# Kernel optimization log

Measured on AMD Instinct MI355X. Metric: run time of the kernel, lower is better.

The kernel has to match this reference:

```python
import jax, jax.numpy as jnp
import numpy as np

# Model dims (Gemma-class)
B, T, HID = 1, 3072, 2048
H, KH, D = 16, 8, 128          # q heads, kv heads, head_dim
WIN = 1024                     # sliding window
EPS = 1e-6
SEQ = 1536                     # two packed sequences of length 1536


def _rms(x, w):
    # torch nn.RMSNorm: x * rsqrt(mean(x^2) + eps) [* weight]
    var = jnp.mean(x * x, axis=-1, keepdims=True)
    y = x * jax.lax.rsqrt(var + EPS)
    return y if w is None else y * w


def _rotate_half(x):
    x1, x2 = jnp.split(x, 2, axis=-1)
    return jnp.concatenate([-x2, x1], axis=-1)


def _rope(x, cos, sin):
    # x: [B,T,h,D]; cos/sin: [B,T,rd] -> unsqueeze head dim (matches cos.unsqueeze(2))
    c = cos[:, :, None, :]
    s = sin[:, :, None, :]
    rd = cos.shape[-1]
    xr, xp = x[..., :rd], x[..., rd:]
    xr = xr * c + _rotate_half(xr) * s
    return jnp.concatenate([xr, xp], axis=-1)


def _build_mask(cu_seqlens):
    # causal & within sliding window & same packed sequence (matches _sliding_mask)
    idx = jnp.arange(T)
    seg = jnp.searchsorted(cu_seqlens, idx, side='right') - 1
    i = idx[:, None]
    j = idx[None, :]
    return (i >= j) & ((i - j) < WIN) & (seg[:, None] == seg[None, :])


def _attn_layer(x, wq, qn, k, v, wo, cos, sin, mask):
    # x: [B,T,HID]; k,v: [T,KH,D] (possibly shared from an earlier layer)
    q = _rope(_rms((x @ wq).reshape(B, T, H, D), qn), cos, sin).reshape(T, H, D)
    rep = H // k.shape[1]
    kk = jnp.repeat(k, rep, axis=1)   # GQA: repeat_interleave over head dim
    vv = jnp.repeat(v, rep, axis=1)
    s = jnp.einsum('qhd,khd->hqk', q, kk)          # scale = 1.0 (as in source)
    s = jnp.where(mask, s, jnp.asarray(-1e30, s.dtype))
    p = jax.nn.softmax(s, axis=-1)
    o = jnp.einsum('hqk,khd->qhd', p, vv).reshape(B, T, H * D)
    return o @ wo


def setup_inputs() -> dict:
    key = jax.random.key(0)
    ks = jax.random.split(key, 10)
    hidden_states = jax.random.normal(ks[0], (B, T, HID), jnp.float32)
    # RoPE tables with per-packed-sequence position resets
    pos = jnp.concatenate([jnp.arange(SEQ), jnp.arange(SEQ)]).astype(jnp.float32)
    inv = 1.0 / (10000.0 ** (jnp.arange(0, D, 2, dtype=jnp.float32) / D))
    fr = pos[:, None] * inv[None, :]
    emb = jnp.concatenate([fr, fr], axis=-1)     # [T, D]
    cos = jnp.cos(emb)[None]                     # [1, T, D]
    sin = jnp.sin(emb)[None]
    w = lambda k, sh: 0.02 * jax.random.normal(k, sh, jnp.float32)
    return {
        'hidden_states': hidden_states,
        'cos': cos, 'sin': sin,
        'wq0': w(ks[1], (HID, H * D)), 'wk0': w(ks[2], (HID, KH * D)),
        'wv0': w(ks[3], (HID, KH * D)), 'wo0': w(ks[4], (H * D, HID)),
        'qn0': 1.0 + 0.01 * jax.random.normal(ks[5], (D,), jnp.float32),
        'kn0': 1.0 + 0.01 * jax.random.normal(ks[6], (D,), jnp.float32),
        'wq1': w(ks[7], (HID, H * D)), 'wo1': w(ks[8], (H * D, HID)),
        'qn1': 1.0 + 0.01 * jax.random.normal(ks[9], (D,), jnp.float32),
        'cu_seqlens': jnp.array([0, SEQ, T], dtype=jnp.int32),
    }


def reference(hidden_states, cos, sin, wq0, wk0, wv0, wo0, qn0, kn0, wq1, wo1, qn1, cu_seqlens):
    mask = _build_mask(cu_seqlens)
    # Layer 0: source layer -> computes and stores K/V
    k = _rope(_rms((hidden_states @ wk0).reshape(B, T, KH, D), kn0), cos, sin).reshape(T, KH, D)
    v = _rms((hidden_states @ wv0).reshape(B, T, KH, D), None).reshape(T, KH, D)
    out0 = _attn_layer(hidden_states, wq0, qn0, k, v, wo0, cos, sin, mask)
    # Layer 1: KV-shared layer -> reuses layer 0's K/V (skips k/v projections)
    out1 = _attn_layer(out0, wq1, qn1, k, v, wo1, cos, sin, mask)
    return out1
```

## Files before the change

kernel.cpp:

```cpp
#include <hip/hip_runtime.h>
#include <hip/hip_bf16.h>

#define T_TOK 3072
#define HIDDEN 2048
#define NHQ 16
#define NHKV 8
#define DH 128
#define WINDOW 1024
#define KVN 1024

typedef __attribute__((ext_vector_type(4))) float f32x4;
typedef __attribute__((ext_vector_type(8))) short bf16x8;
typedef __attribute__((ext_vector_type(8))) unsigned short ushort8;
typedef __attribute__((ext_vector_type(4))) unsigned short ushort4v;

__device__ __forceinline__ unsigned short f2bf(float f) {
  union { float fv; unsigned u; } v; v.fv = f;
  unsigned r = v.u + 0x7fffu + ((v.u >> 16) & 1u);
  return (unsigned short)(r >> 16);
}
__device__ __forceinline__ float bf2f(unsigned short h) {
  union { unsigned u; float f; } v; v.u = ((unsigned)h) << 16;
  return v.f;
}
__device__ __forceinline__ void split2(float f, unsigned short& hi, unsigned short& lo) {
  hi = f2bf(f);
  lo = f2bf(f - bf2f(hi));
}

__global__ __launch_bounds__(256) void cvt_split(const float* __restrict__ x,
                                                 unsigned short* __restrict__ yh,
                                                 unsigned short* __restrict__ yl, int n) {
  int i = (blockIdx.x * 256 + threadIdx.x) * 4;
  if (i >= n) return;
  f32x4 v = *(const f32x4*)(x + i);
  ushort4v oh, ol;
#pragma unroll
  for (int j = 0; j < 4; ++j) {
    unsigned short h, l;
    split2(v[j], h, l);
    oh[j] = h; ol[j] = l;
  }
  *(ushort4v*)(yh + i) = oh;
  *(ushort4v*)(yl + i) = ol;
}

__global__ __launch_bounds__(256) void transpose_qkv(const float* __restrict__ wq0,
                                                     const float* __restrict__ wk0,
                                                     const float* __restrict__ wv0,
                                                     unsigned short* __restrict__ Wth,
                                                     unsigned short* __restrict__ Wtl) {
  __shared__ float tile[32][33];
  const int K = HIDDEN;
  int id = blockIdx.x;
  const float* W; int N, local; size_t dstoff;
  if (id < 4096)      { W = wq0; N = 2048; local = id;        dstoff = 0; }
  else if (id < 6144) { W = wk0; N = 1024; local = id - 4096; dstoff = (size_t)2048 * K; }
  else                { W = wv0; N = 1024; local = id - 6144; dstoff = (size_t)3072 * K; }
  int ntc = N / 32;
  int bn = (local % ntc) * 32, bk = (local / ntc) * 32;
  int tx = threadIdx.x & 31, ty = threadIdx.x >> 5;
#pragma unroll
  for (int i = 0; i < 4; ++i)
    tile[ty + i * 8][tx] = W[(size_t)(bk + ty + i * 8) * N + bn + tx];
  __syncthreads();
#pragma unroll
  for (int i = 0; i < 4; ++i) {
    unsigned short h, l;
    split2(tile[tx][ty + i * 8], h, l);
    Wth[dstoff + (size_t)(bn + ty + i * 8) * K + bk + tx] = h;
    Wtl[dstoff + (size_t)(bn + ty + i * 8) * K + bk + tx] = l;
  }
}

__global__ __launch_bounds__(256) void transpose_w_split(const float* __restrict__ W,
                                                         unsigned short* __restrict__ Wth,
                                                         unsigned short* __restrict__ Wtl,
                                                         int K, int N) {
  __shared__ float tile[32][33];
  int bn = blockIdx.x * 32, bk = blockIdx.y * 32;
  int tx = threadIdx.x & 31, ty = threadIdx.x >> 5;
#pragma unroll
  for (int i = 0; i < 4; ++i)
    tile[ty + i * 8][tx] = W[(size_t)(bk + ty + i * 8) * N + bn + tx];
  __syncthreads();
#pragma unroll
  for (int i = 0; i < 4; ++i) {
    unsigned short h, l;
    split2(tile[tx][ty + i * 8], h, l);
    Wth[(size_t)(bn + ty + i * 8) * K + bk + tx] = h;
    if (Wtl) Wtl[(size_t)(bn + ty + i * 8) * K + bk + tx] = l;
  }
}

__global__ __launch_bounds__(256) void transpose_u16(const unsigned short* __restrict__ src,
                                                     unsigned short* __restrict__ dst,
                                                     int R, int C) {
  __shared__ unsigned short tile[32][33];
  int bc = blockIdx.x * 32, br = blockIdx.y * 32;
  int tx = threadIdx.x & 31, ty = threadIdx.x >> 5;
#pragma unroll
  for (int i = 0; i < 4; ++i)
    tile[ty + i * 8][tx] = src[(size_t)(br + ty + i * 8) * C + bc + tx];
  __syncthreads();
#pragma unroll
  for (int i = 0; i < 4; ++i)
    dst[(size_t)(bc + ty + i * 8) * R + br + tx] = tile[tx][ty + i * 8];
}

#define GSLOT(lane) ((((lane) & 3) + 4 - (((lane) >> 3) & 3)) & 3)

template <int OUT>
__global__ __launch_bounds__(256) void gemm3_128(const unsigned short* __restrict__ Ah,
                                                 const unsigned short* __restrict__ Al,
                                                 const unsigned short* __restrict__ Bh,
                                                 const unsigned short* __restrict__ Bl,
                                                 float* __restrict__ Cq,
                                                 float* __restrict__ Ckv,
                                                 unsigned short* __restrict__ Ch,
                                                 unsigned short* __restrict__ Cl,
                                                 int strd, int M, int N, int K) {
  __shared__ unsigned short ah_lds[128 * 32];
  __shared__ unsigned short al_lds[128 * 32];
  __shared__ unsigned short bh_lds[128 * 32];
  __shared__ unsigned short bl_lds[128 * 32];
  const int tid = threadIdx.x, lane = tid & 63, wave = tid >> 6;
  const int wr = (wave >> 1) * 64, wc = (wave & 1) * 64;
  const int g = lane >> 4, r16 = lane & 15;
  int nwg = gridDim.x * gridDim.y;
  int id = blockIdx.y * gridDim.x + blockIdx.x;
  int nid = (id & 7) * (nwg >> 3) + (id >> 3);
  const int bm = nid % gridDim.x, bn = nid / gridDim.x;
  f32x4 acc[4][4];
#pragma unroll
  for (int i = 0; i < 4; ++i)
#pragma unroll
    for (int j = 0; j < 4; ++j) acc[i][j] = (f32x4){0.f, 0.f, 0.f, 0.f};

  const unsigned short* AhB = Ah + (size_t)bm * 128 * K;
  const unsigned short* AlB = Al + (size_t)bm * 128 * K;
  const unsigned short* BhB = Bh + (size_t)bn * 128 * K;
  const unsigned short* BlB = Bl + (size_t)bn * 128 * K;

  const int slg = GSLOT(lane) * 8;
  const int sr = ((r16 >> 1) & 3);

  for (int kt = 0; kt < K; kt += 32) {
    __syncthreads();
#pragma unroll
    for (int c = 0; c < 2; ++c) {
      size_t goff = (size_t)(wave * 32 + c * 16 + (lane >> 2)) * K + kt + slg;
      int loff = (wave * 2 + c) * 512;
      __builtin_amdgcn_global_load_lds(
          (const __attribute__((address_space(1))) unsigned int*)(AhB + goff),
          (__attribute__((address_space(3))) unsigned int*)(ah_lds + loff), 16, 0, 0);
      __builtin_amdgcn_global_load_lds(
          (const __attribute__((address_space(1))) unsigned int*)(AlB + goff),
          (__attribute__((address_space(3))) unsigned int*)(al_lds + loff), 16, 0, 0);
      __builtin_amdgcn_global_load_lds(
          (const __attribute__((address_space(1))) unsigned int*)(BhB + goff),
          (__attribute__((address_space(3))) unsigned int*)(bh_lds + loff), 16, 0, 0);
      __builtin_amdgcn_global_load_lds(
          (const __attribute__((address_space(1))) unsigned int*)(BlB + goff),
          (__attribute__((address_space(3))) unsigned int*)(bl_lds + loff), 16, 0, 0);
    }
    __syncthreads();
    bf16x8 ahf[4], alf[4], bhf[4], blf[4];
    int sa = ((g + sr) & 3) * 8;
#pragma unroll
    for (int i = 0; i < 4; ++i) {
      ahf[i] = *(const bf16x8*)&ah_lds[(wr + i * 16 + r16) * 32 + sa];
      alf[i] = *(const bf16x8*)&al_lds[(wr + i * 16 + r16) * 32 + sa];
      bhf[i] = *(const bf16x8*)&bh_lds[(wc + i * 16 + r16) * 32 + sa];
      blf[i] = *(const bf16x8*)&bl_lds[(wc + i * 16 + r16) * 32 + sa];
    }
#pragma unroll
    for (int i = 0; i < 4; ++i)
#pragma unroll
      for (int j = 0; j < 4; ++j) {
        acc[i][j] = __builtin_amdgcn_mfma_f32_16x16x32_bf16(ahf[i], bhf[j], acc[i][j], 0, 0, 0);
        acc[i][j] = __builtin_amdgcn_mfma_f32_16x16x32_bf16(ahf[i], blf[j], acc[i][j], 0, 0, 0);
        acc[i][j] = __builtin_amdgcn_mfma_f32_16x16x32_bf16(alf[i], bhf[j], acc[i][j], 0, 0, 0);
      }
  }

#pragma unroll
  for (int i = 0; i < 4; ++i) {
    int row = bm * 128 + wr + i * 16 + g * 4;
#pragma unroll
    for (int j = 0; j < 4; ++j) {
      int colg = bn * 128 + wc + j * 16 + r16;
      if (OUT == 0) {
        float* Cb; int cc;
        if (colg < 2048) { Cb = Cq; cc = colg; } else { Cb = Ckv; cc = colg - 2048; }
#pragma unroll
        for (int r = 0; r < 4; ++r)
          Cb[(size_t)(row + r) * strd + cc] = acc[i][j][r];
      } else {
#pragma unroll
        for (int r = 0; r < 4; ++r) {
          unsigned short h, l;
          split2(acc[i][j][r], h, l);
          Ch[(size_t)(row + r) * N + colg] = h;
          Cl[(size_t)(row + r) * N + colg] = l;
        }
      }
    }
  }
}

__global__ __launch_bounds__(256) void gemm3_96(const unsigned short* __restrict__ Ah,
                                                const unsigned short* __restrict__ Al,
                                                const unsigned short* __restrict__ Bh,
                                                const unsigned short* __restrict__ Bl,
                                                float* __restrict__ Cf,
                                                int M, int N, int K) {
  __shared__ unsigned short ah_lds[96 * 32];
  __shared__ unsigned short al_lds[96 * 32];
  __shared__ unsigned short bh_lds[128 * 32];
  __shared__ unsigned short bl_lds[128 * 32];
  const int tid = threadIdx.x, lane = tid & 63, wave = tid >> 6;
  const int wr = (wave >> 1) * 48, wc = (wave & 1) * 64;
  const int g = lane >> 4, r16 = lane & 15;
  int nwg = gridDim.x * gridDim.y;
  int id = blockIdx.y * gridDim.x + blockIdx.x;
  int nid = (id & 7) * (nwg >> 3) + (id >> 3);
  const int bm = nid % gridDim.x, bn = nid / gridDim.x;
  f32x4 acc[3][4];
#pragma unroll
  for (int i = 0; i < 3; ++i)
#pragma unroll
    for (int j = 0; j < 4; ++j) acc[i][j] = (f32x4){0.f, 0.f, 0.f, 0.f};

  const unsigned short* AhB = Ah + (size_t)bm * 96 * K;
  const unsigned short* AlB = Al + (size_t)bm * 96 * K;
  const unsigned short* BhB = Bh + (size_t)bn * 128 * K;
  const unsigned short* BlB = Bl + (size_t)bn * 128 * K;

  const int slg = GSLOT(lane) * 8;
  const int sr = ((r16 >> 1) & 3);

  for (int kt = 0; kt < K; kt += 32) {
    __syncthreads();
    {
      int c = wave;
      size_t goff = (size_t)(c * 16 + (lane >> 2)) * K + kt + slg;
      __builtin_amdgcn_global_load_lds(
          (const __attribute__((address_space(1))) unsigned int*)(AhB + goff),
          (__attribute__((address_space(3))) unsigned int*)(ah_lds + c * 512), 16, 0, 0);
      __builtin_amdgcn_global_load_lds(
          (const __attribute__((address_space(1))) unsigned int*)(AlB + goff),
          (__attribute__((address_space(3))) unsigned int*)(al_lds + c * 512), 16, 0, 0);
      if (wave < 2) {
        int c2 = 4 + wave;
        size_t goff2 = (size_t)(c2 * 16 + (lane >> 2)) * K + kt + slg;
        __builtin_amdgcn_global_load_lds(
            (const __attribute__((address_space(1))) unsigned int*)(AhB + goff2),
            (__attribute__((address_space(3))) unsigned int*)(ah_lds + c2 * 512), 16, 0, 0);
        __builtin_amdgcn_global_load_lds(
            (const __attribute__((address_space(1))) unsigned int*)(AlB + goff2),
            (__attribute__((address_space(3))) unsigned int*)(al_lds + c2 * 512), 16, 0, 0);
      }
    }
#pragma unroll
    for (int c = 0; c < 2; ++c) {
      size_t goff = (size_t)(wave * 32 + c * 16 + (lane >> 2)) * K + kt + slg;
      int loff = (wave * 2 + c) * 512;
      __builtin_amdgcn_global_load_lds(
          (const __attribute__((address_space(1))) unsigned int*)(BhB + goff),
          (__attribute__((address_space(3))) unsigned int*)(bh_lds + loff), 16, 0, 0);
      __builtin_amdgcn_global_load_lds(
          (const __attribute__((address_space(1))) unsigned int*)(BlB + goff),
          (__attribute__((address_space(3))) unsigned int*)(bl_lds + loff), 16, 0, 0);
    }
    __syncthreads();
    bf16x8 ahf[3], alf[3], bhf[4], blf[4];
    int sa = ((g + sr) & 3) * 8;
#pragma unroll
    for (int i = 0; i < 3; ++i) {
      ahf[i] = *(const bf16x8*)&ah_lds[(wr + i * 16 + r16) * 32 + sa];
      alf[i] = *(const bf16x8*)&al_lds[(wr + i * 16 + r16) * 32 + sa];
    }
#pragma unroll
    for (int j = 0; j < 4; ++j) {
      bhf[j] = *(const bf16x8*)&bh_lds[(wc + j * 16 + r16) * 32 + sa];
      blf[j] = *(const bf16x8*)&bl_lds[(wc + j * 16 + r16) * 32 + sa];
    }
#pragma unroll
    for (int i = 0; i < 3; ++i)
#pragma unroll
      for (int j = 0; j < 4; ++j) {
        acc[i][j] = __builtin_amdgcn_mfma_f32_16x16x32_bf16(ahf[i], bhf[j], acc[i][j], 0, 0, 0);
        acc[i][j] = __builtin_amdgcn_mfma_f32_16x16x32_bf16(ahf[i], blf[j], acc[i][j], 0, 0, 0);
        acc[i][j] = __builtin_amdgcn_mfma_f32_16x16x32_bf16(alf[i], bhf[j], acc[i][j], 0, 0, 0);
      }
  }

#pragma unroll
  for (int i = 0; i < 3; ++i) {
    int row = bm * 96 + wr + i * 16 + g * 4;
#pragma unroll
    for (int j = 0; j < 4; ++j) {
      int col = bn * 128 + wc + j * 16 + r16;
#pragma unroll
      for (int r = 0; r < 4; ++r)
        Cf[(size_t)(row + r) * N + col] = acc[i][j][r];
    }
  }
}

__global__ __launch_bounds__(256) void gemm1_96(const unsigned short* __restrict__ Ah,
                                                const unsigned short* __restrict__ Bh,
                                                float* __restrict__ Cf,
                                                int M, int N, int K) {
  __shared__ unsigned short ah_lds[96 * 32];
  __shared__ unsigned short bh_lds[128 * 32];
  const int tid = threadIdx.x, lane = tid & 63, wave = tid >> 6;
  const int wr = (wave >> 1) * 48, wc = (wave & 1) * 64;
  const int g = lane >> 4, r16 = lane & 15;
  int nwg = gridDim.x * gridDim.y;
  int id = blockIdx.y * gridDim.x + blockIdx.x;
  int nid = (id & 7) * (nwg >> 3) + (id >> 3);
  const int bm = nid % gridDim.x, bn = nid / gridDim.x;
  f32x4 acc[3][4];
#pragma unroll
  for (int i = 0; i < 3; ++i)
#pragma unroll
    for (int j = 0; j < 4; ++j) acc[i][j] = (f32x4){0.f, 0.f, 0.f, 0.f};

  const unsigned short* AhB = Ah + (size_t)bm * 96 * K;
  const unsigned short* BhB = Bh + (size_t)bn * 128 * K;

  const int slg = GSLOT(lane) * 8;
  const int sr = ((r16 >> 1) & 3);

  for (int kt = 0; kt < K; kt += 32) {
    __syncthreads();
    {
      int c = wave;
      size_t goff = (size_t)(c * 16 + (lane >> 2)) * K + kt + slg;
      __builtin_amdgcn_global_load_lds(
          (const __attribute__((address_space(1))) unsigned int*)(AhB + goff),
          (__attribute__((address_space(3))) unsigned int*)(ah_lds + c * 512), 16, 0, 0);
      if (wave < 2) {
        int c2 = 4 + wave;
        size_t goff2 = (size_t)(c2 * 16 + (lane >> 2)) * K + kt + slg;
        __builtin_amdgcn_global_load_lds(
            (const __attribute__((address_space(1))) unsigned int*)(AhB + goff2),
            (__attribute__((address_space(3))) unsigned int*)(ah_lds + c2 * 512), 16, 0, 0);
      }
    }
#pragma unroll
    for (int c = 0; c < 2; ++c) {
      size_t goff = (size_t)(wave * 32 + c * 16 + (lane >> 2)) * K + kt + slg;
      __builtin_amdgcn_global_load_lds(
          (const __attribute__((address_space(1))) unsigned int*)(BhB + goff),
          (__attribute__((address_space(3))) unsigned int*)(bh_lds + (wave * 2 + c) * 512), 16, 0, 0);
    }
    __syncthreads();
    bf16x8 ahf[3], bhf[4];
    int sa = ((g + sr) & 3) * 8;
#pragma unroll
    for (int i = 0; i < 3; ++i)
      ahf[i] = *(const bf16x8*)&ah_lds[(wr + i * 16 + r16) * 32 + sa];
#pragma unroll
    for (int j = 0; j < 4; ++j)
      bhf[j] = *(const bf16x8*)&bh_lds[(wc + j * 16 + r16) * 32 + sa];
#pragma unroll
    for (int i = 0; i < 3; ++i)
#pragma unroll
      for (int j = 0; j < 4; ++j)
        acc[i][j] = __builtin_amdgcn_mfma_f32_16x16x32_bf16(ahf[i], bhf[j], acc[i][j], 0, 0, 0);
  }

#pragma unroll
  for (int i = 0; i < 3; ++i) {
    int row = bm * 96 + wr + i * 16 + g * 4;
#pragma unroll
    for (int j = 0; j < 4; ++j) {
      int col = bn * 128 + wc + j * 16 + r16;
#pragma unroll
      for (int r = 0; r < 4; ++r)
        Cf[(size_t)(row + r) * N + col] = acc[i][j][r];
    }
  }
}

__global__ __launch_bounds__(256) void rms_kv(const float* __restrict__ X,
                                              const float* __restrict__ kn,
                                              const float* __restrict__ cosp,
                                              const float* __restrict__ sinp,
                                              unsigned short* __restrict__ kh,
                                              unsigned short* __restrict__ kl,
                                              unsigned short* __restrict__ vh) {
  const int half = T_TOK * NHKV / 4;
  bool isV = (int)blockIdx.x >= half;
  int bid = isV ? blockIdx.x - half : blockIdx.x;
  int row = bid * 4 + (threadIdx.x >> 6);
  int lane = threadIdx.x & 63;
  int t = row >> 3, hh_ = row & 7;
  const float* x = X + (size_t)t * HIDDEN + (isV ? KVN : 0) + (size_t)hh_ * DH;
  float x1 = x[lane], x2 = x[lane + 64];
  float ss = x1 * x1 + x2 * x2;
#pragma unroll
  for (int m = 1; m < 64; m <<= 1) ss += __shfl_xor(ss, m, 64);
  float inv = rsqrtf(ss * (1.0f / 128.0f) + 1e-6f);
  float y1 = x1 * inv, y2 = x2 * inv;
  if (!isV) {
    y1 *= kn[lane]; y2 *= kn[lane + 64];
    float c1 = cosp[t * DH + lane], s1 = sinp[t * DH + lane];
    float c2 = cosp[t * DH + lane + 64], s2 = sinp[t * DH + lane + 64];
    float o1 = y1 * c1 - y2 * s1;
    float o2 = y2 * c2 + y1 * s2;
    unsigned short h, l;
    split2(o1, h, l);
    kh[(size_t)row * DH + lane] = h;
    kl[(size_t)row * DH + lane] = l;
    split2(o2, h, l);
    kh[(size_t)row * DH + lane + 64] = h;
    kl[(size_t)row * DH + lane + 64] = l;
  } else {
    vh[(size_t)row * DH + lane] = f2bf(y1);
    vh[(size_t)row * DH + lane + 64] = f2bf(y2);
  }
}

template <int WRITE_LO>
__global__ __launch_bounds__(384) void attn3(const float* __restrict__ Qf,
                                             const float* __restrict__ qnw,
                                             const float* __restrict__ cosp,
                                             const float* __restrict__ sinp,
                                             const unsigned short* __restrict__ Kh,
                                             const unsigned short* __restrict__ Kl,
                                             const unsigned short* __restrict__ Vth,
                                             unsigned short* __restrict__ Oh,
                                             unsigned short* __restrict__ Ol,
                                             const int* __restrict__ cu, int ncu) {
  __shared__ unsigned short kh_lds[32][136];
  __shared__ unsigned short kl_lds[32][136];
  __shared__ unsigned short vh_lds[144][40];
  __shared__ unsigned short ph_lds[6][16][40];

  int id = blockIdx.y * gridDim.x + blockIdx.x;
  int nid = (id & 7) * 64 + (id >> 3);
  const int qt = nid & 31, h = nid >> 5;
  const int qbase = qt * 96;
  const int kvh = h >> 1;
  const int tid = threadIdx.x, lane = tid & 63, wave = tid >> 6;
  const int g = lane >> 4, r16 = lane & 15;

  for (int i = tid; i < 16 * 40; i += 384) {
    int rr = i / 40, cc = i % 40;
    vh_lds[128 + rr][cc] = (rr == 0) ? (unsigned short)0x3F80 : (unsigned short)0;
  }

  bf16x8 aqh[4], aql[4];
  {
    int q_r = qbase + wave * 16 + r16;
    const float* xq = Qf + (size_t)q_r * HIDDEN + h * DH;
    float xv[4][8];
    float ss = 0.f;
#pragma unroll
    for (int ks = 0; ks < 4; ++ks) {
      f32x4 a = *(const f32x4*)(xq + ks * 32 + g * 8);
      f32x4 b = *(const f32x4*)(xq + ks * 32 + g * 8 + 4);
#pragma unroll
      for (int j = 0; j < 4; ++j) { xv[ks][j] = a[j]; xv[ks][4 + j] = b[j]; }
#pragma unroll
      for (int j = 0; j < 8; ++j) ss += xv[ks][j] * xv[ks][j];
    }
    ss += __shfl_xor(ss, 16, 64);
    ss += __shfl_xor(ss, 32, 64);
    float inv = rsqrtf(ss * (1.0f / 128.0f) + 1e-6f);
    float y[4][8];
#pragma unroll
    for (int ks = 0; ks < 4; ++ks) {
      f32x4 w0 = *(const f32x4*)(qnw + ks * 32 + g * 8);
      f32x4 w1 = *(const f32x4*)(qnw + ks * 32 + g * 8 + 4);
#pragma unroll
      for (int j = 0; j < 4; ++j) {
        y[ks][j] = xv[ks][j] * inv * w0[j];
        y[ks][4 + j] = xv[ks][4 + j] * inv * w1[j];
      }
    }
    const float* cb = cosp + (size_t)q_r * DH;
    const float* sb = sinp + (size_t)q_r * DH;
#pragma unroll
    for (int ks = 0; ks < 4; ++ks) {
      bf16x8 th, tl;
#pragma unroll
      for (int j2 = 0; j2 < 2; ++j2) {
        int col = ks * 32 + g * 8 + j2 * 4;
        f32x4 cv = *(const f32x4*)(cb + col);
        f32x4 sv = *(const f32x4*)(sb + col);
#pragma unroll
        for (int j = 0; j < 4; ++j) {
          float o;
          if (ks < 2) o = y[ks][j2 * 4 + j] * cv[j] - y[ks + 2][j2 * 4 + j] * sv[j];
          else        o = y[ks][j2 * 4 + j] * cv[j] + y[ks - 2][j2 * 4 + j] * sv[j];
          unsigned short hx, lx;
          split2(o, hx, lx);
          th[j2 * 4 + j] = (short)hx;
          tl[j2 * 4 + j] = (short)lx;
        }
      }
      aqh[ks] = th; aql[ks] = tl;
    }
  }

  int ssr[4];
#pragma unroll
  for (int r = 0; r < 4; ++r) {
    int q_r = qbase + wave * 16 + g * 4 + r;
    int s = 0;
    for (int i = 1; i < ncu; ++i) { int v = cu[i]; if (v <= q_r) s = v; }
    ssr[r] = s;
  }
  int ss_base = 0;
  for (int i = 1; i < ncu; ++i) { int v = cu[i]; if (v <= qbase) ss_base = v; }

  float m_r[4] = {-1e30f, -1e30f, -1e30f, -1e30f};
  f32x4 oacc[8];
#pragma unroll
  for (int db = 0; db < 8; ++db) oacc[db] = (f32x4){0.f, 0.f, 0.f, 0.f};
  f32x4 oaccL = (f32x4){0.f, 0.f, 0.f, 0.f};

  int lo = qbase - WINDOW + 1;
  if (lo < ss_base) lo = ss_base;
  if (lo < 0) lo = 0;
  int kt0 = lo & ~31;
  int ktend = qbase + 95;

  const bool stager = tid < 256;
  const int krow = (tid & 255) >> 3, kc = tid & 7;
  const int vd = (tid & 255) >> 1, vhalf = (tid & 1) * 16;
  const int qmin = qbase + wave * 16;
  const int sw0 = ((kc + 2 * (krow & 15)) & 15) * 16;
  const int sw1 = ((kc + 8 + 2 * (krow & 15)) & 15) * 16;

  ushort8 rkh0, rkh1, rkl0, rkl1, rvh0, rvh1;
  auto loadTile = [&](int kt) {
    if (!stager) return;
    size_t goff = ((size_t)(kt + krow) * NHKV + kvh) * DH + kc * 8;
    rkh0 = *(const ushort8*)(Kh + goff);
    rkh1 = *(const ushort8*)(Kh + goff + 64);
    rkl0 = *(const ushort8*)(Kl + goff);
    rkl1 = *(const ushort8*)(Kl + goff + 64);
    size_t voff = ((size_t)kvh * DH + vd) * T_TOK + kt + vhalf;
    rvh0 = *(const ushort8*)(Vth + voff);
    rvh1 = *(const ushort8*)(Vth + voff + 8);
  };
  auto writeTile = [&]() {
    if (!stager) return;
    char* kbh = (char*)&kh_lds[krow][0];
    char* kbl = (char*)&kl_lds[krow][0];
    *(ushort8*)(kbh + sw0) = rkh0;
    *(ushort8*)(kbh + sw1) = rkh1;
    *(ushort8*)(kbl + sw0) = rkl0;
    *(ushort8*)(kbl + sw1) = rkl1;
    *(ushort8*)&vh_lds[vd][vhalf] = rvh0;
    *(ushort8*)&vh_lds[vd][vhalf + 8] = rvh1;
  };

  loadTile(kt0);
  writeTile();
  __syncthreads();

  for (int kt = kt0; kt <= ktend; kt += 32) {
    const bool hasNext = (kt + 32 <= ktend);
    if (hasNext) loadTile(kt + 32);

    f32x4 s0 = (f32x4){0.f, 0.f, 0.f, 0.f}, s1 = (f32x4){0.f, 0.f, 0.f, 0.f};
    {
      const char* kb0h = (const char*)&kh_lds[r16][0];
      const char* kb1h = (const char*)&kh_lds[16 + r16][0];
      const char* kb0l = (const char*)&kl_lds[r16][0];
      const char* kb1l = (const char*)&kl_lds[16 + r16][0];
#pragma unroll
      for (int ks = 0; ks < 4; ++ks) {
        int sl = ((ks * 4 + g + 2 * r16) & 15) * 16;
        bf16x8 bh0 = *(const bf16x8*)(kb0h + sl);
        bf16x8 bh1 = *(const bf16x8*)(kb1h + sl);
        bf16x8 bl0 = *(const bf16x8*)(kb0l + sl);
        bf16x8 bl1 = *(const bf16x8*)(kb1l + sl);
        s0 = __builtin_amdgcn_mfma_f32_16x16x32_bf16(aqh[ks], bh0, s0, 0, 0, 0);
        s0 = __builtin_amdgcn_mfma_f32_16x16x32_bf16(aqh[ks], bl0, s0, 0, 0, 0);
        s0 = __builtin_amdgcn_mfma_f32_16x16x32_bf16(aql[ks], bh0, s0, 0, 0, 0);
        s1 = __builtin_amdgcn_mfma_f32_16x16x32_bf16(aqh[ks], bh1, s1, 0, 0, 0);
        s1 = __builtin_amdgcn_mfma_f32_16x16x32_bf16(aqh[ks], bl1, s1, 0, 0, 0);
        s1 = __builtin_amdgcn_mfma_f32_16x16x32_bf16(aql[ks], bh1, s1, 0, 0, 0);
      }
    }

    float sv0_[4], sv1_[4], mt_[4];
    bool ok0_[4], ok1_[4];
    bool interior = (kt + 31 <= qmin) && (kt >= qmin + 16 - WINDOW) &&
                    __all(kt >= ssr[3]);
    if (interior) {
#pragma unroll
      for (int r = 0; r < 4; ++r) {
        ok0_[r] = ok1_[r] = true;
        sv0_[r] = s0[r]; sv1_[r] = s1[r];
      }
    } else {
#pragma unroll
      for (int r = 0; r < 4; ++r) {
        int q_r = qmin + g * 4 + r;
        int k0 = kt + r16, k1 = k0 + 16;
        ok0_[r] = (k0 <= q_r) && (k0 > q_r - WINDOW) && (k0 >= ssr[r]);
        ok1_[r] = (k1 <= q_r) && (k1 > q_r - WINDOW) && (k1 >= ssr[r]);
        sv0_[r] = ok0_[r] ? s0[r] : -1e30f;
        sv1_[r] = ok1_[r] ? s1[r] : -1e30f;
      }
    }
#pragma unroll
    for (int r = 0; r < 4; ++r) {
      float mt = fmaxf(sv0_[r], sv1_[r]);
#pragma unroll
      for (int mm = 1; mm < 16; mm <<= 1) mt = fmaxf(mt, __shfl_xor(mt, mm, 64));
      mt_[r] = mt;
    }
    float grow = fmaxf(fmaxf(mt_[0] - m_r[0], mt_[1] - m_r[1]),
                       fmaxf(mt_[2] - m_r[2], mt_[3] - m_r[3]));
    if (!__all(grow <= 8.0f)) {
#pragma unroll
      for (int r = 0; r < 4; ++r) {
        float mnew = fmaxf(m_r[r], mt_[r]);
        float alpha = __expf(m_r[r] - mnew);
        m_r[r] = mnew;
#pragma unroll
        for (int db = 0; db < 8; ++db) oacc[db][r] *= alpha;
        oaccL[r] *= alpha;
      }
    }
#pragma unroll
    for (int r = 0; r < 4; ++r) {
      float p0v = ok0_[r] ? __expf(sv0_[r] - m_r[r]) : 0.f;
      float p1v = ok1_[r] ? __expf(sv1_[r] - m_r[r]) : 0.f;
      ph_lds[wave][g * 4 + r][r16] = f2bf(p0v);
      ph_lds[wave][g * 4 + r][16 + r16] = f2bf(p1v);
    }

    bf16x8 pah = *(const bf16x8*)&ph_lds[wave][r16][g * 8];
#pragma unroll
    for (int db = 0; db < 8; ++db) {
      bf16x8 vfh = *(const bf16x8*)&vh_lds[db * 16 + r16][g * 8];
      oacc[db] = __builtin_amdgcn_mfma_f32_16x16x32_bf16(pah, vfh, oacc[db], 0, 0, 0);
    }
    {
      bf16x8 vfo = *(const bf16x8*)&vh_lds[128 + r16][g * 8];
      oaccL = __builtin_amdgcn_mfma_f32_16x16x32_bf16(pah, vfo, oaccL, 0, 0, 0);
    }

    __syncthreads();
    if (hasNext) writeTile();
    __syncthreads();
  }

#pragma unroll
  for (int r = 0; r < 4; ++r) {
    int q_r = qbase + wave * 16 + g * 4 + r;
    float lsum = __shfl(oaccL[r], lane & 48, 64);
    float invl = 1.f / lsum;
#pragma unroll
    for (int db = 0; db < 8; ++db) {
      float ov = oacc[db][r] * invl;
      unsigned short hh, ll;
      split2(ov, hh, ll);
      Oh[(size_t)q_r * (NHQ * DH) + h * DH + db * 16 + r16] = hh;
      if (WRITE_LO) Ol[(size_t)q_r * (NHQ * DH) + h * DH + db * 16 + r16] = ll;
    }
  }
}

extern "C" void kernel_launch(void* const* d_in, const int* in_sizes, int n_in,
                              void* d_out, int out_size, void* d_ws, size_t ws_size,
                              hipStream_t stream) {
  const float* hidden = (const float*)d_in[0];
  const float* cosp   = (const float*)d_in[1];
  const float* sinp   = (const float*)d_in[2];
  const float* wq0    = (const float*)d_in[3];
  const float* wk0    = (const float*)d_in[4];
  const float* wv0    = (const float*)d_in[5];
  const float* wo0    = (const float*)d_in[6];
  const float* qn0    = (const float*)d_in[7];
  const float* kn0    = (const float*)d_in[8];
  const float* wq1    = (const float*)d_in[9];
  const float* wo1    = (const float*)d_in[10];
  const float* qn1    = (const float*)d_in[11];
  const int*   cu     = (const int*)d_in[12];
  int ncu = in_sizes[12];
  (void)n_in; (void)out_size; (void)ws_size;

  const int nX = T_TOK * HIDDEN;

  char* p = (char*)d_ws;
  auto alloc = [&](size_t bytes) { char* r = p; p += (bytes + 255) & ~255ull; return r; };

  float*          c32q  = (float*)alloc((size_t)T_TOK * HIDDEN * 4);
  float*          c32kv = (float*)alloc((size_t)T_TOK * HIDDEN * 4);
  unsigned short* xh    = (unsigned short*)alloc((size_t)T_TOK * HIDDEN * 2);
  unsigned short* xl    = (unsigned short*)alloc((size_t)T_TOK * HIDDEN * 2);
  unsigned short* wth   = (unsigned short*)alloc((size_t)2 * HIDDEN * HIDDEN * 2);
  unsigned short* wtl   = (unsigned short*)alloc((size_t)2 * HIDDEN * HIDDEN * 2);
  unsigned short* kh    = (unsigned short*)alloc((size_t)T_TOK * KVN * 2);
  unsigned short* kl    = (unsigned short*)alloc((size_t)T_TOK * KVN * 2);
  unsigned short* vh    = (unsigned short*)alloc((size_t)T_TOK * KVN * 2);
  unsigned short* vth   = (unsigned short*)alloc((size_t)T_TOK * KVN * 2);

  unsigned short* wo0sh = wth;
  unsigned short* wo0sl = wtl;
  unsigned short* wq1th = wth + (size_t)HIDDEN * HIDDEN;
  unsigned short* wq1tl = wtl + (size_t)HIDDEN * HIDDEN;
  unsigned short* W01th = (unsigned short*)c32q;
  unsigned short* W01tl = W01th + (size_t)HIDDEN * HIDDEN;
  unsigned short* wo1t  = wth;

  cvt_split<<<nX / 1024, 256, 0, stream>>>(hidden, xh, xl, nX);
  transpose_qkv<<<8192, 256, 0, stream>>>(wq0, wk0, wv0, wth, wtl);
  gemm3_128<0><<<dim3(T_TOK / 128, 4096 / 128), 256, 0, stream>>>(
      xh, xl, wth, wtl, c32q, c32kv, nullptr, nullptr, HIDDEN, T_TOK, 4096, HIDDEN);
  cvt_split<<<(HIDDEN * HIDDEN) / 1024, 256, 0, stream>>>(wo0, wo0sh, wo0sl, HIDDEN * HIDDEN);
  transpose_w_split<<<dim3(HIDDEN / 32, HIDDEN / 32), 256, 0, stream>>>(wq1, wq1th, wq1tl, HIDDEN, HIDDEN);
  rms_kv<<<2 * T_TOK * NHKV / 4, 256, 0, stream>>>(c32kv, kn0, cosp, sinp, kh, kl, vh);
  transpose_u16<<<dim3(KVN / 32, T_TOK / 32), 256, 0, stream>>>(vh, vth, T_TOK, KVN);
  attn3<1><<<dim3(32, 16), 384, 0, stream>>>(c32q, qn0, cosp, sinp, kh, kl, vth, xh, xl, cu, ncu);
  gemm3_128<2><<<dim3(HIDDEN / 128, HIDDEN / 128), 256, 0, stream>>>(
      wq1th, wq1tl, wo0sh, wo0sl, nullptr, nullptr, W01th, W01tl, HIDDEN, HIDDEN, HIDDEN, HIDDEN);
  gemm3_96<<<dim3(T_TOK / 96, HIDDEN / 128), 256, 0, stream>>>(
      xh, xl, W01th, W01tl, c32kv, T_TOK, HIDDEN, HIDDEN);
  transpose_w_split<<<dim3(HIDDEN / 32, HIDDEN / 32), 256, 0, stream>>>(wo1, wo1t, nullptr, HIDDEN, HIDDEN);
  attn3<0><<<dim3(32, 16), 384, 0, stream>>>(c32kv, qn1, cosp, sinp, kh, kl, vth, xh, nullptr, cu, ncu);
  gemm1_96<<<dim3(T_TOK / 96, HIDDEN / 128), 256, 0, stream>>>(xh, wo1t, (float*)d_out, T_TOK, HIDDEN, HIDDEN);
}
```

Measured before the change: 668.3 us.

## Fuse weight/input prep kernels, add 64-row GEMM for W01, set MFMA priority

Merges the input split, QKV transpose, wo0 split and wq1 transpose into one prep launch, with a separate workspace for each weight, which cuts launch count and the ordering constraints from aliased buffers. Replaces the 128x128 tile for the 2048x2048 weight-product GEMM with a 64x128 tile, giving more workgroups to fill the CUs. Adds s_setprio around the MFMA loops in attention, and simplifies the wo1 transpose to write only the high bf16 part. The changes are independent and add more kernel code to maintain.

```diff
diff --git a/kernel.cpp b/kernel.cpp
--- a/kernel.cpp
+++ b/kernel.cpp
@@ -28,35 +28,51 @@
   lo = f2bf(f - bf2f(hi));
 }
 
-__global__ __launch_bounds__(256) void cvt_split(const float* __restrict__ x,
-                                                 unsigned short* __restrict__ yh,
-                                                 unsigned short* __restrict__ yl, int n) {
-  int i = (blockIdx.x * 256 + threadIdx.x) * 4;
-  if (i >= n) return;
-  f32x4 v = *(const f32x4*)(x + i);
-  ushort4v oh, ol;
-#pragma unroll
-  for (int j = 0; j < 4; ++j) {
-    unsigned short h, l;
-    split2(v[j], h, l);
-    oh[j] = h; ol[j] = l;
-  }
-  *(ushort4v*)(yh + i) = oh;
-  *(ushort4v*)(yl + i) = ol;
-}
-
-__global__ __launch_bounds__(256) void transpose_qkv(const float* __restrict__ wq0,
-                                                     const float* __restrict__ wk0,
-                                                     const float* __restrict__ wv0,
-                                                     unsigned short* __restrict__ Wth,
-                                                     unsigned short* __restrict__ Wtl) {
+__global__ __launch_bounds__(256) void prep(const float* __restrict__ hidden,
+                                            const float* __restrict__ wq0,
+                                            const float* __restrict__ wk0,
+                                            const float* __restrict__ wv0,
+                                            const float* __restrict__ wo0,
+                                            const float* __restrict__ wq1,
+                                            unsigned short* __restrict__ xh,
+                                            unsigned short* __restrict__ xl,
+                                            unsigned short* __restrict__ wqkvh,
+                                            unsigned short* __restrict__ wqkvl,
+                                            unsigned short* __restrict__ wo0sh,
+                                            unsigned short* __restrict__ wo0sl,
+                                            unsigned short* __restrict__ wq1th,
+                                            unsigned short* __restrict__ wq1tl) {
   __shared__ float tile[32][33];
   const int K = HIDDEN;
   int id = blockIdx.x;
-  const float* W; int N, local; size_t dstoff;
-  if (id < 4096)      { W = wq0; N = 2048; local = id;        dstoff = 0; }
-  else if (id < 6144) { W = wk0; N = 1024; local = id - 4096; dstoff = (size_t)2048 * K; }
-  else                { W = wv0; N = 1024; local = id - 6144; dstoff = (size_t)3072 * K; }
+  if (id < 6144 || (id >= 14336 && id < 18432)) {
+    const float* src; unsigned short *dh, *dl; int local;
+    if (id < 6144) { src = hidden; dh = xh; dl = xl; local = id; }
+    else           { src = wo0; dh = wo0sh; dl = wo0sl; local = id - 14336; }
+    int i = (local * 256 + threadIdx.x) * 4;
+    f32x4 v = *(const f32x4*)(src + i);
+    ushort4v oh, ol;
+#pragma unroll
+    for (int j = 0; j < 4; ++j) {
+      unsigned short h, l;
+      split2(v[j], h, l);
+      oh[j] = h; ol[j] = l;
+    }
+    *(ushort4v*)(dh + i) = oh;
+    *(ushort4v*)(dl + i) = ol;
+    return;
+  }
+  const float* W; int N, local; unsigned short *Dh, *Dl; size_t dstoff;
+  if (id < 14336) {
+    int lid = id - 6144;
+    if (lid < 4096)      { W = wq0; N = 2048; local = lid;        dstoff = 0; }
+    else if (lid < 6144) { W = wk0; N = 1024; local = lid - 4096; dstoff = (size_t)2048 * K; }
+    else                 { W = wv0; N = 1024; local = lid - 6144; dstoff = (size_t)3072 * K; }
+    Dh = wqkvh; Dl = wqkvl;
+  } else {
+    W = wq1; N = 2048; local = id - 18432; dstoff = 0;
+    Dh = wq1th; Dl = wq1tl;
+  }
   int ntc = N / 32;
   int bn = (local % ntc) * 32, bk = (local / ntc) * 32;
   int tx = threadIdx.x & 31, ty = threadIdx.x >> 5;
@@ -68,15 +84,14 @@
   for (int i = 0; i < 4; ++i) {
     unsigned short h, l;
     split2(tile[tx][ty + i * 8], h, l);
-    Wth[dstoff + (size_t)(bn + ty + i * 8) * K + bk + tx] = h;
-    Wtl[dstoff + (size_t)(bn + ty + i * 8) * K + bk + tx] = l;
-  }
-}
-
-__global__ __launch_bounds__(256) void transpose_w_split(const float* __restrict__ W,
-                                                         unsigned short* __restrict__ Wth,
-                                                         unsigned short* __restrict__ Wtl,
-                                                         int K, int N) {
+    Dh[dstoff + (size_t)(bn + ty + i * 8) * K + bk + tx] = h;
+    Dl[dstoff + (size_t)(bn + ty + i * 8) * K + bk + tx] = l;
+  }
+}
+
+__global__ __launch_bounds__(256) void transpose_w_hi(const float* __restrict__ W,
+                                                      unsigned short* __restrict__ Wth,
+                                                      int K, int N) {
   __shared__ float tile[32][33];
   int bn = blockIdx.x * 32, bk = blockIdx.y * 32;
   int tx = threadIdx.x & 31, ty = threadIdx.x >> 5;
@@ -85,12 +100,8 @@
     tile[ty + i * 8][tx] = W[(size_t)(bk + ty + i * 8) * N + bn + tx];
   __syncthreads();
 #pragma unroll
-  for (int i = 0; i < 4; ++i) {
-    unsigned short h, l;
-    split2(tile[tx][ty + i * 8], h, l);
-    Wth[(size_t)(bn + ty + i * 8) * K + bk + tx] = h;
-    if (Wtl) Wtl[(size_t)(bn + ty + i * 8) * K + bk + tx] = l;
-  }
+  for (int i = 0; i < 4; ++i)
+    Wth[(size_t)(bn + ty + i * 8) * K + bk + tx] = f2bf(tile[tx][ty + i * 8]);
 }
 
 __global__ __launch_bounds__(256) void transpose_u16(const unsigned short* __restrict__ src,
@@ -110,15 +121,12 @@
 
 #define GSLOT(lane) ((((lane) & 3) + 4 - (((lane) >> 3) & 3)) & 3)
 
-template <int OUT>
 __global__ __launch_bounds__(256) void gemm3_128(const unsigned short* __restrict__ Ah,
                                                  const unsigned short* __restrict__ Al,
                                                  const unsigned short* __restrict__ Bh,
                                                  const unsigned short* __restrict__ Bl,
                                                  float* __restrict__ Cq,
                                                  float* __restrict__ Ckv,
-                                                 unsigned short* __restrict__ Ch,
-                                                 unsigned short* __restrict__ Cl,
                                                  int strd, int M, int N, int K) {
   __shared__ unsigned short ah_lds[128 * 32];
   __shared__ unsigned short al_lds[128 * 32];
@@ -190,20 +198,104 @@
 #pragma unroll
     for (int j = 0; j < 4; ++j) {
       int colg = bn * 128 + wc + j * 16 + r16;
-      if (OUT == 0) {
-        float* Cb; int cc;
-        if (colg < 2048) { Cb = Cq; cc = colg; } else { Cb = Ckv; cc = colg - 2048; }
-#pragma unroll
-        for (int r = 0; r < 4; ++r)
-          Cb[(size_t)(row + r) * strd + cc] = acc[i][j][r];
-      } else {
-#pragma unroll
-        for (int r = 0; r < 4; ++r) {
-          unsigned short h, l;
-          split2(acc[i][j][r], h, l);
-          Ch[(size_t)(row + r) * N + colg] = h;
-          Cl[(size_t)(row + r) * N + colg] = l;
-        }
+      float* Cb; int cc;
+      if (colg < 2048) { Cb = Cq; cc = colg; } else { Cb = Ckv; cc = colg - 2048; }
+#pragma unroll
+      for (int r = 0; r < 4; ++r)
+        Cb[(size_t)(row + r) * strd + cc] = acc[i][j][r];
+    }
+  }
+}
+
+__global__ __launch_bounds__(256) void gemm3_64(const unsigned short* __restrict__ Ah,
+                                                const unsigned short* __restrict__ Al,
+                                                const unsigned short* __restrict__ Bh,
+                                                const unsigned short* __restrict__ Bl,
+                                                unsigned short* __restrict__ Ch,
+                                                unsigned short* __restrict__ Cl,
+                                                int M, int N, int K) {
+  __shared__ unsigned short ah_lds[64 * 32];
+  __shared__ unsigned short al_lds[64 * 32];
+  __shared__ unsigned short bh_lds[128 * 32];
+  __shared__ unsigned short bl_lds[128 * 32];
+  const int tid = threadIdx.x, lane = tid & 63, wave = tid >> 6;
+  const int wr = (wave >> 1) * 32, wc = (wave & 1) * 64;
+  const int g = lane >> 4, r16 = lane & 15;
+  int nwg = gridDim.x * gridDim.y;
+  int id = blockIdx.y * gridDim.x + blockIdx.x;
+  int nid = (id & 7) * (nwg >> 3) + (id >> 3);
+  const int bm = nid % gridDim.x, bn = nid / gridDim.x;
+  f32x4 acc[2][4];
+#pragma unroll
+  for (int i = 0; i < 2; ++i)
+#pragma unroll
+    for (int j = 0; j < 4; ++j) acc[i][j] = (f32x4){0.f, 0.f, 0.f, 0.f};
+
+  const unsigned short* AhB = Ah + (size_t)bm * 64 * K;
+  const unsigned short* AlB = Al + (size_t)bm * 64 * K;
+  const unsigned short* BhB = Bh + (size_t)bn * 128 * K;
+  const unsigned short* BlB = Bl + (size_t)bn * 128 * K;
+
+  const int slg = GSLOT(lane) * 8;
+  const int sr = ((r16 >> 1) & 3);
+
+  for (int kt = 0; kt < K; kt += 32) {
+    __syncthreads();
+    {
+      size_t goff = (size_t)(wave * 16 + (lane >> 2)) * K + kt + slg;
+      __builtin_amdgcn_global_load_lds(
+          (const __attribute__((address_space(1))) unsigned int*)(AhB + goff),
+          (__attribute__((address_space(3))) unsigned int*)(ah_lds + wave * 512), 16, 0, 0);
+      __builtin_amdgcn_global_load_lds(
+          (const __attribute__((address_space(1))) unsigned int*)(AlB + goff),
+          (__attribute__((address_space(3))) unsigned int*)(al_lds + wave * 512), 16, 0, 0);
+    }
+#pragma unroll
+    for (int c = 0; c < 2; ++c) {
+      size_t goff = (size_t)(wave * 32 + c * 16 + (lane >> 2)) * K + kt + slg;
+      int loff = (wave * 2 + c) * 512;
+      __builtin_amdgcn_global_load_lds(
+          (const __attribute__((address_space(1))) unsigned int*)(BhB + goff),
+          (__attribute__((address_space(3))) unsigned int*)(bh_lds + loff), 16, 0, 0);
+      __builtin_amdgcn_global_load_lds(
+          (const __attribute__((address_space(1))) unsigned int*)(BlB + goff),
+          (__attribute__((address_space(3))) unsigned int*)(bl_lds + loff), 16, 0, 0);
+    }
+    __syncthreads();
+    bf16x8 ahf[2], alf[2], bhf[4], blf[4];
+    int sa = ((g + sr) & 3) * 8;
+#pragma unroll
+    for (int i = 0; i < 2; ++i) {
+      ahf[i] = *(const bf16x8*)&ah_lds[(wr + i * 16 + r16) * 32 + sa];
+      alf[i] = *(const bf16x8*)&al_lds[(wr + i * 16 + r16) * 32 + sa];
+    }
+#pragma unroll
+    for (int j = 0; j < 4; ++j) {
+      bhf[j] = *(const bf16x8*)&bh_lds[(wc + j * 16 + r16) * 32 + sa];
+      blf[j] = *(const bf16x8*)&bl_lds[(wc + j * 16 + r16) * 32 + sa];
+    }
+#pragma unroll
+    for (int i = 0; i < 2; ++i)
+#pragma unroll
+      for (int j = 0; j < 4; ++j) {
+        acc[i][j] = __builtin_amdgcn_mfma_f32_16x16x32_bf16(ahf[i], bhf[j], acc[i][j], 0, 0, 0);
+        acc[i][j] = __builtin_amdgcn_mfma_f32_16x16x32_bf16(ahf[i], blf[j], acc[i][j], 0, 0, 0);
+        acc[i][j] = __builtin_amdgcn_mfma_f32_16x16x32_bf16(alf[i], bhf[j], acc[i][j], 0, 0, 0);
+      }
+  }
+
+#pragma unroll
+  for (int i = 0; i < 2; ++i) {
+    int row = bm * 64 + wr + i * 16 + g * 4;
+#pragma unroll
+    for (int j = 0; j < 4; ++j) {
+      int col = bn * 128 + wc + j * 16 + r16;
+#pragma unroll
+      for (int r = 0; r < 4; ++r) {
+        unsigned short h, l;
+        split2(acc[i][j][r], h, l);
+        Ch[(size_t)(row + r) * N + col] = h;
+        Cl[(size_t)(row + r) * N + col] = l;
       }
     }
   }
@@ -576,6 +668,7 @@
       const char* kb1h = (const char*)&kh_lds[16 + r16][0];
       const char* kb0l = (const char*)&kl_lds[r16][0];
       const char* kb1l = (const char*)&kl_lds[16 + r16][0];
+      __builtin_amdgcn_s_setprio(1);
 #pragma unroll
       for (int ks = 0; ks < 4; ++ks) {
         int sl = ((ks * 4 + g + 2 * r16) & 15) * 16;
@@ -590,6 +683,7 @@
         s1 = __builtin_amdgcn_mfma_f32_16x16x32_bf16(aqh[ks], bl1, s1, 0, 0, 0);
         s1 = __builtin_amdgcn_mfma_f32_16x16x32_bf16(aql[ks], bh1, s1, 0, 0, 0);
       }
+      __builtin_amdgcn_s_setprio(0);
     }
 
     float sv0_[4], sv1_[4], mt_[4];
@@ -642,6 +736,7 @@
     }
 
     bf16x8 pah = *(const bf16x8*)&ph_lds[wave][r16][g * 8];
+    __builtin_amdgcn_s_setprio(1);
 #pragma unroll
     for (int db = 0; db < 8; ++db) {
       bf16x8 vfh = *(const bf16x8*)&vh_lds[db * 16 + r16][g * 8];
@@ -651,6 +746,7 @@
       bf16x8 vfo = *(const bf16x8*)&vh_lds[128 + r16][g * 8];
       oaccL = __builtin_amdgcn_mfma_f32_16x16x32_bf16(pah, vfo, oaccL, 0, 0, 0);
     }
+    __builtin_amdgcn_s_setprio(0);
 
     __syncthreads();
     if (hasNext) writeTile();
@@ -692,44 +788,48 @@
   int ncu = in_sizes[12];
   (void)n_in; (void)out_size; (void)ws_size;
 
-  const int nX = T_TOK * HIDDEN;
-
   char* p = (char*)d_ws;
   auto alloc = [&](size_t bytes) { char* r = p; p += (bytes + 255) & ~255ull; return r; };
 
+  unsigned short* wqkvh = (unsigned short*)alloc((size_t)2 * HIDDEN * HIDDEN * 2);
+  unsigned short* wqkvl = (unsigned short*)alloc((size_t)2 * HIDDEN * HIDDEN * 2);
+  unsigned short* wo0sh = (unsigned short*)alloc((size_t)HIDDEN * HIDDEN * 2);
+  unsigned short* wo0sl = (unsigned short*)alloc((size_t)HIDDEN * HIDDEN * 2);
+  unsigned short* wq1th = (unsigned short*)alloc((size_t)HIDDEN * HIDDEN * 2);
+  unsigned short* wq1tl = (unsigned short*)alloc((size_t)HIDDEN * HIDDEN * 2);
   float*          c32q  = (float*)alloc((size_t)T_TOK * HIDDEN * 4);
   float*          c32kv = (float*)alloc((size_t)T_TOK * HIDDEN * 4);
   unsigned short* xh    = (unsigned short*)alloc((size_t)T_TOK * HIDDEN * 2);
   unsigned short* xl    = (unsigned short*)alloc((size_t)T_TOK * HIDDEN * 2);
-  unsigned short* wth   = (unsigned short*)alloc((size_t)2 * HIDDEN * HIDDEN * 2);
-  unsigned short* wtl   = (unsigned short*)alloc((size_t)2 * HIDDEN * HIDDEN * 2);
   unsigned short* kh    = (unsigned short*)alloc((size_t)T_TOK * KVN * 2);
   unsigned short* kl    = (unsigned short*)alloc((size_t)T_TOK * KVN * 2);
   unsigned short* vh    = (unsigned short*)alloc((size_t)T_TOK * KVN * 2);
   unsigned short* vth   = (unsigned short*)alloc((size_t)T_TOK * KVN * 2);
 
-  unsigned short* wo0sh = wth;
-  unsigned short* wo0sl = wtl;
-  unsigned short* wq1th = wth + (size_t)HIDDEN * HIDDEN;
-  unsigned short* wq1tl = wtl + (size_t)HIDDEN * HIDDEN;
   unsigned short* W01th = (unsigned short*)c32q;
   unsigned short* W01tl = W01th + (size_t)HIDDEN * HIDDEN;
-  unsigned short* wo1t  = wth;
-
-  cvt_split<<<nX / 1024, 256, 0, stream>>>(hidden, xh, xl, nX);
-  transpose_qkv<<<8192, 256, 0, stream>>>(wq0, wk0, wv0, wth, wtl);
-  gemm3_128<0><<<dim3(T_TOK / 128, 4096 / 128), 256, 0, stream>>>(
-      xh, xl, wth, wtl, c32q, c32kv, nullptr, nullptr, HIDDEN, T_TOK, 4096, HIDDEN);
-  cvt_split<<<(HIDDEN * HIDDEN) / 1024, 256, 0, stream>>>(wo0, wo0sh, wo0sl, HIDDEN * HIDDEN);
-  transpose_w_split<<<dim3(HIDDEN / 32, HIDDEN / 32), 256, 0, stream>>>(wq1, wq1th, wq1tl, HIDDEN, HIDDEN);
+  unsigned short* wo1t  = W01tl + (size_t)HIDDEN * HIDDEN;
+
+  prep<<<22528, 256, 0, stream>>>(hidden, wq0, wk0, wv0, wo0, wq1,
+                                  xh, xl, wqkvh, wqkvl, wo0sh, wo0sl, wq1th, wq1tl);
+
+  gemm3_128<<<dim3(T_TOK / 128, 4096 / 128), 256, 0, stream>>>(
+      xh, xl, wqkvh, wqkvl, c32q, c32kv, HIDDEN, T_TOK, 4096, HIDDEN);
+
   rms_kv<<<2 * T_TOK * NHKV / 4, 256, 0, stream>>>(c32kv, kn0, cosp, sinp, kh, kl, vh);
   transpose_u16<<<dim3(KVN / 32, T_TOK / 32), 256, 0, stream>>>(vh, vth, T_TOK, KVN);
+
   attn3<1><<<dim3(32, 16), 384, 0, stream>>>(c32q, qn0, cosp, sinp, kh, kl, vth, xh, xl, cu, ncu);
-  gemm3_128<2><<<dim3(HIDDEN / 128, HIDDEN / 128), 256, 0, stream>>>(
-      wq1th, wq1tl, wo0sh, wo0sl, nullptr, nullptr, W01th, W01tl, HIDDEN, HIDDEN, HIDDEN, HIDDEN);
+
+  gemm3_64<<<dim3(HIDDEN / 64, HIDDEN / 128), 256, 0, stream>>>(
+      wq1th, wq1tl, wo0sh, wo0sl, W01th, W01tl, HIDDEN, HIDDEN, HIDDEN);
+
+  transpose_w_hi<<<dim3(HIDDEN / 32, HIDDEN / 32), 256, 0, stream>>>(wo1, wo1t, HIDDEN, HIDDEN);
+
   gemm3_96<<<dim3(T_TOK / 96, HIDDEN / 128), 256, 0, stream>>>(
       xh, xl, W01th, W01tl, c32kv, T_TOK, HIDDEN, HIDDEN);
-  transpose_w_split<<<dim3(HIDDEN / 32, HIDDEN / 32), 256, 0, stream>>>(wo1, wo1t, nullptr, HIDDEN, HIDDEN);
+
   attn3<0><<<dim3(32, 16), 384, 0, stream>>>(c32kv, qn1, cosp, sinp, kh, kl, vth, xh, nullptr, cu, ncu);
+
   gemm1_96<<<dim3(T_TOK / 96, HIDDEN / 128), 256, 0, stream>>>(xh, wo1t, (float*)d_out, T_TOK, HIDDEN, HIDDEN);
 }
```

After: 659.5 us. Within noise of the previous version (-1.3%).
